# Optimization experiments

Hardware: AMD Instinct MI355X
Metric: run time of the kernel (lower is better)

## Reference

```python
import jax, jax.numpy as jnp
import numpy as np

IN_CHS = 128
NUM_HEADS = 4
WIN = 7
N = WIN * WIN            # 49 tokens per window
QKDIM = 128              # ceil(in_chs/num_groups/num_heads)*num_heads
HEAD_DIM = QKDIM // NUM_HEADS
SCALE = HEAD_DIM ** -0.5
B = 4096                 # batch * num_windows


def _relative_position_index(win_h, win_w):
    coords = np.stack(np.meshgrid(np.arange(win_h), np.arange(win_w), indexing='ij'))  # [2,h,w]
    cf = coords.reshape(2, -1)                      # [2, N]
    rc = (cf[:, :, None] - cf[:, None, :]).transpose(1, 2, 0).astype(np.int64)  # [N,N,2]
    rc[:, :, 0] += win_h - 1
    rc[:, :, 1] += win_w - 1
    rc[:, :, 0] *= 2 * win_w - 1
    return rc.sum(-1)                               # [N, N]


def setup_inputs() -> dict:
    key = jax.random.key(0)
    ks = jax.random.split(key, 8)
    x = jax.random.normal(ks[0], (B, N, IN_CHS), dtype=jnp.float32)
    qk_w = jax.random.normal(ks[1], (2 * QKDIM, IN_CHS), dtype=jnp.float32) * 0.02
    qk_b = jnp.zeros((2 * QKDIM,), dtype=jnp.float32)
    v_w = jax.random.normal(ks[2], (IN_CHS, IN_CHS), dtype=jnp.float32) * 0.02
    v_b = jnp.zeros((IN_CHS,), dtype=jnp.float32)
    proj_w = jax.random.normal(ks[3], (IN_CHS, IN_CHS), dtype=jnp.float32) * 0.02
    proj_b = jnp.zeros((IN_CHS,), dtype=jnp.float32)
    bias_table = jax.random.normal(ks[4], ((2 * WIN - 1) * (2 * WIN - 1), NUM_HEADS), dtype=jnp.float32) * 0.02
    rel_idx = jnp.asarray(_relative_position_index(WIN, WIN))  # [N,N] int64
    return {"x": x, "qk_w": qk_w, "qk_b": qk_b, "v_w": v_w, "v_b": v_b,
            "proj_w": proj_w, "proj_b": proj_b, "bias_table": bias_table,
            "rel_idx": rel_idx}


def reference(x, qk_w, qk_b, v_w, v_b, proj_w, proj_b, bias_table, rel_idx):
    Bn, Nn, C = x.shape
    # fused q/k projection: [B,N,2*qkdim] -> q,k each [B,H,N,d]
    qk = (x @ qk_w.T + qk_b).reshape(Bn, Nn, 2, NUM_HEADS, HEAD_DIM)
    q = qk[:, :, 0].transpose(0, 2, 1, 3)
    k = qk[:, :, 1].transpose(0, 2, 1, 3)
    v = (x @ v_w.T + v_b).reshape(Bn, Nn, NUM_HEADS, -1).transpose(0, 2, 1, 3)
    # windowed QK^T with gathered relative-position bias
    attn = jnp.einsum('bhnd,bhmd->bhnm', q * SCALE, k)
    bias = bias_table[rel_idx.reshape(-1)].reshape(Nn, Nn, NUM_HEADS).transpose(2, 0, 1)
    attn = jax.nn.softmax(attn + bias[None], axis=-1)
    out = jnp.einsum('bhnm,bhmd->bhnd', attn, v).transpose(0, 2, 1, 3).reshape(Bn, Nn, -1)
    return out @ proj_w.T + proj_b
```

## Files before the change

### kernel.cpp

```cpp
#include <hip/hip_runtime.h>
#include <hip/hip_bf16.h>

typedef __attribute__((ext_vector_type(8))) __bf16 bf16x8;
typedef __attribute__((ext_vector_type(4))) short short4v;
typedef __attribute__((ext_vector_type(4))) float f32x4;

#define MFMA(a,b,c) __builtin_amdgcn_mfma_f32_16x16x32_bf16((a),(b),(c),0,0,0)
#define MFMA16(a,b,c) __builtin_amdgcn_mfma_f32_16x16x16bf16_1k((a),(b),(c),0,0,0)

#define XB 0u
#define VT 16384u
#define OB 32768u

static __device__ __forceinline__ unsigned short f2u(float x) {
  return __builtin_bit_cast(unsigned short, static_cast<__bf16>(x));
}
static __device__ __forceinline__ unsigned long long pack4(float a, float b, float c, float d) {
  union { __bf16 h[4]; unsigned long long u; } z;
  z.h[0] = static_cast<__bf16>(a);
  z.h[1] = static_cast<__bf16>(b);
  z.h[2] = static_cast<__bf16>(c);
  z.h[3] = static_cast<__bf16>(d);
  return z.u;
}
static __device__ __forceinline__ unsigned long long pack4v(f32x4 v) {
  return pack4(v[0], v[1], v[2], v[3]);
}
static __device__ __forceinline__ short4v pack4s(float a, float b, float c, float d) {
  union { __bf16 h[4]; short4v s; } z;
  z.h[0] = static_cast<__bf16>(a);
  z.h[1] = static_cast<__bf16>(b);
  z.h[2] = static_cast<__bf16>(c);
  z.h[3] = static_cast<__bf16>(d);
  return z.s;
}
static __device__ __forceinline__ short4v pack4sv(f32x4 v) {
  return pack4s(v[0], v[1], v[2], v[3]);
}
static __device__ __forceinline__ unsigned sw256(unsigned row, unsigned colb) {
  return (row << 8) + (colb ^ ((row & 7u) << 4));
}
static __device__ __forceinline__ unsigned sw128(unsigned row, unsigned colb) {
  return (row << 7) + (colb ^ ((row & 7u) << 4));
}

__global__ void rsa_prep(const float* __restrict__ qk_w, const float* __restrict__ v_w,
                         const float* __restrict__ proj_w, const float* __restrict__ bias_table,
                         unsigned short* __restrict__ wqk, unsigned short* __restrict__ wv,
                         unsigned short* __restrict__ wp, float* __restrict__ biasNN) {
  const float QSCALE = 0.17677669529663687f * 1.4426950408889634f;
  const float LOG2E = 1.4426950408889634f;
  int t = blockIdx.x * blockDim.x + threadIdx.x;
  int stride = gridDim.x * blockDim.x;
  for (int i = t; i < 256 * 128; i += stride) {
    float v = qk_w[i];
    if (i < 128 * 128) v *= QSCALE;
    wqk[i] = f2u(v);
  }
  for (int i = t; i < 128 * 128; i += stride) wv[i] = f2u(v_w[i]);
  for (int i = t; i < 128 * 128; i += stride) wp[i] = f2u(proj_w[i]);
  for (int i = t; i < 4 * 64 * 64; i += stride) {
    int h = i >> 12, r = (i >> 6) & 63, m = i & 63;
    float v = -1e9f;
    if (r < 49 && m < 49) {
      int ri = r / 7, rj = r - ri * 7, mi = m / 7, mj = m - mi * 7;
      int rel = (ri - mi + 6) * 13 + (rj - mj + 6);
      v = bias_table[rel * 4 + h];
    }
    biasNN[i] = v * LOG2E;
  }
}

__global__ __launch_bounds__(256, 3) void rsa_main(
    const float* __restrict__ x, const float* __restrict__ qk_bias,
    const float* __restrict__ v_bias, const float* __restrict__ proj_bias,
    const unsigned short* __restrict__ wqk, const unsigned short* __restrict__ wv,
    const unsigned short* __restrict__ wp, const float* __restrict__ biasNN,
    float* __restrict__ out) {
  __shared__ __align__(16) unsigned char LDS[49152];
  const int tid = threadIdx.x;
  const int w = tid >> 6;
  const int lane = tid & 63;
  const int c = lane & 15;
  const int g = lane >> 4;
  const int b = blockIdx.x;
  const float QBSCALE = 0.17677669529663687f * 1.4426950408889634f;

  {
    const f32x4* xp = reinterpret_cast<const f32x4*>(x + (size_t)b * 6272);
    for (int i = tid; i < 1568; i += 256) {
      f32x4 v = xp[i];
      unsigned row = (unsigned)i >> 5, c4 = (unsigned)i & 31u;
      *reinterpret_cast<unsigned long long*>(LDS + XB + sw256(row, c4 * 8)) = pack4v(v);
    }
    for (int i = tid; i < 480; i += 256) {
      unsigned row = 49 + ((unsigned)i >> 5), c4 = (unsigned)i & 31u;
      *reinterpret_cast<unsigned long long*>(LDS + XB + sw256(row, c4 * 8)) = 0ull;
    }
  }
  __syncthreads();

  f32x4 qacc[2][4], kacc[2][4];
  {
#pragma unroll
    for (int kt = 0; kt < 2; ++kt) {
      f32x4 qb4 = *reinterpret_cast<const f32x4*>(qk_bias + (2 * w + kt) * 16 + g * 4);
      qb4[0] *= QBSCALE; qb4[1] *= QBSCALE; qb4[2] *= QBSCALE; qb4[3] *= QBSCALE;
      f32x4 kb4 = *reinterpret_cast<const f32x4*>(qk_bias + 128 + (2 * w + kt) * 16 + g * 4);
#pragma unroll
      for (int nt = 0; nt < 4; ++nt) { qacc[kt][nt] = qb4; kacc[kt][nt] = kb4; }
    }
    __builtin_amdgcn_s_setprio(1);
#pragma unroll
    for (int ks = 0; ks < 4; ++ks) {
      bf16x8 wq0 = *reinterpret_cast<const bf16x8*>(wqk + ((2 * w) * 16 + c) * 128 + ks * 32 + g * 8);
      bf16x8 wq1 = *reinterpret_cast<const bf16x8*>(wqk + ((2 * w + 1) * 16 + c) * 128 + ks * 32 + g * 8);
      bf16x8 wk0 = *reinterpret_cast<const bf16x8*>(wqk + (128 + (2 * w) * 16 + c) * 128 + ks * 32 + g * 8);
      bf16x8 wk1 = *reinterpret_cast<const bf16x8*>(wqk + (128 + (2 * w + 1) * 16 + c) * 128 + ks * 32 + g * 8);
#pragma unroll
      for (int nt = 0; nt < 4; ++nt) {
        bf16x8 xf = *reinterpret_cast<const bf16x8*>(LDS + XB + sw256(nt * 16 + c, (ks * 32 + g * 8) * 2));
        qacc[0][nt] = MFMA(wq0, xf, qacc[0][nt]);
        qacc[1][nt] = MFMA(wq1, xf, qacc[1][nt]);
        kacc[0][nt] = MFMA(wk0, xf, kacc[0][nt]);
        kacc[1][nt] = MFMA(wk1, xf, kacc[1][nt]);
      }
    }
    __builtin_amdgcn_s_setprio(0);
  }
  short4v q16[2][4], k16[2][4];
#pragma unroll
  for (int kt = 0; kt < 2; ++kt)
#pragma unroll
    for (int nt = 0; nt < 4; ++nt) {
      q16[kt][nt] = pack4sv(qacc[kt][nt]);
      k16[kt][nt] = pack4sv(kacc[kt][nt]);
    }

  __builtin_amdgcn_s_setprio(1);
#pragma unroll
  for (int ci = 0; ci < 2; ++ci) {
    const int ch = (2 * w + ci) * 16 + c;
    const float vb = v_bias[ch];
    f32x4 vacc[4];
#pragma unroll
    for (int mt = 0; mt < 4; ++mt) vacc[mt] = f32x4{vb, vb, vb, vb};
#pragma unroll
    for (int ks = 0; ks < 4; ++ks) {
      bf16x8 bw = *reinterpret_cast<const bf16x8*>(wv + ch * 128 + ks * 32 + g * 8);
#pragma unroll
      for (int mt = 0; mt < 4; ++mt) {
        bf16x8 xf = *reinterpret_cast<const bf16x8*>(LDS + XB + sw256(mt * 16 + c, (ks * 32 + g * 8) * 2));
        vacc[mt] = MFMA(xf, bw, vacc[mt]);
      }
    }
#pragma unroll
    for (int mt = 0; mt < 4; ++mt)
      *reinterpret_cast<unsigned long long*>(LDS + VT + sw128(ch, (mt * 16 + g * 4) * 2)) =
          pack4v(vacc[mt]);
  }
  __builtin_amdgcn_s_setprio(0);

  short4v pk[4][4];
#pragma unroll
  for (int rt = 0; rt < 4; ++rt) {
    f32x4 bbr[4];
    {
      const float* bp = biasNN + ((w * 64 + rt * 16 + c) << 6);
#pragma unroll
      for (int mt = 0; mt < 4; ++mt)
        bbr[mt] = *reinterpret_cast<const f32x4*>(bp + mt * 16 + g * 4);
    }
    f32x4 s[4];
    __builtin_amdgcn_s_setprio(1);
#pragma unroll
    for (int mt = 0; mt < 4; ++mt)
      s[mt] = MFMA16(k16[1][mt], q16[1][rt], MFMA16(k16[0][mt], q16[0][rt], bbr[mt]));
    __builtin_amdgcn_s_setprio(0);
    float v[16];
#pragma unroll
    for (int mt = 0; mt < 4; ++mt) {
#pragma unroll
      for (int j = 0; j < 4; ++j) v[mt * 4 + j] = exp2f(s[mt][j]);
    }
    float p0 = (v[0] + v[1]) + (v[2] + v[3]);
    float p1 = (v[4] + v[5]) + (v[6] + v[7]);
    float p2 = (v[8] + v[9]) + (v[10] + v[11]);
    float p3 = (v[12] + v[13]) + (v[14] + v[15]);
    float sum = (p0 + p1) + (p2 + p3);
    sum += __shfl_xor(sum, 16);
    sum += __shfl_xor(sum, 32);
    const float inv = __builtin_amdgcn_rcpf(sum);
#pragma unroll
    for (int mt = 0; mt < 4; ++mt)
      pk[rt][mt] = pack4s(v[mt * 4] * inv, v[mt * 4 + 1] * inv,
                          v[mt * 4 + 2] * inv, v[mt * 4 + 3] * inv);
  }

  f32x4 od[2][4];
  {
    short4v vfrag[2][4];
#pragma unroll
    for (int ct = 0; ct < 2; ++ct)
#pragma unroll
      for (int mt = 0; mt < 4; ++mt)
        vfrag[ct][mt] = *reinterpret_cast<const short4v*>(
            LDS + VT + sw128((2 * w + ct) * 16 + c, (mt * 16 + g * 4) * 2));
#pragma unroll
    for (int ct = 0; ct < 2; ++ct)
#pragma unroll
      for (int rt = 0; rt < 4; ++rt) od[ct][rt] = f32x4{0.f, 0.f, 0.f, 0.f};
    __builtin_amdgcn_s_setprio(1);
#pragma unroll
    for (int mt = 0; mt < 4; ++mt)
#pragma unroll
      for (int ct = 0; ct < 2; ++ct)
#pragma unroll
        for (int rt = 0; rt < 4; ++rt)
          od[ct][rt] = MFMA16(vfrag[ct][mt], pk[rt][mt], od[ct][rt]);
    __builtin_amdgcn_s_setprio(0);
  }

  bf16x8 ap[2][4];
  f32x4 pb4[2];
#pragma unroll
  for (int u = 0; u < 2; ++u) {
    const unsigned short* wrow = wp + ((2 * w + u) * 16 + c) * 128 + g * 8;
#pragma unroll
    for (int ks = 0; ks < 4; ++ks) ap[u][ks] = *reinterpret_cast<const bf16x8*>(wrow + ks * 32);
    pb4[u] = *reinterpret_cast<const f32x4*>(proj_bias + (2 * w + u) * 16 + g * 4);
  }

#pragma unroll
  for (int ct = 0; ct < 2; ++ct)
#pragma unroll
    for (int rt = 0; rt < 4; ++rt)
      *reinterpret_cast<unsigned long long*>(
          LDS + OB + sw256(rt * 16 + c, ((2 * w + ct) * 16 + g * 4) * 2)) = pack4v(od[ct][rt]);
  __syncthreads();

  __builtin_amdgcn_s_setprio(1);
#pragma unroll
  for (int u = 0; u < 2; ++u) {
    f32x4 acc[4];
#pragma unroll
    for (int nt = 0; nt < 4; ++nt) acc[nt] = pb4[u];
#pragma unroll
    for (int ks = 0; ks < 4; ++ks) {
#pragma unroll
      for (int nt = 0; nt < 4; ++nt) {
        bf16x8 bf = *reinterpret_cast<const bf16x8*>(LDS + OB + sw256(nt * 16 + c, (ks * 32 + g * 8) * 2));
        acc[nt] = MFMA(ap[u][ks], bf, acc[nt]);
      }
    }
#pragma unroll
    for (int nt = 0; nt < 4; ++nt) {
      const int tok = nt * 16 + c;
      if (tok < 49) {
        *reinterpret_cast<f32x4*>(out + ((size_t)b * 49 + tok) * 128 + (2 * w + u) * 16 + g * 4) = acc[nt];
      }
    }
  }
  __builtin_amdgcn_s_setprio(0);
}

extern "C" void kernel_launch(void* const* d_in, const int* in_sizes, int n_in,
                              void* d_out, int out_size, void* d_ws, size_t ws_size,
                              hipStream_t stream) {
  const float* x          = (const float*)d_in[0];
  const float* qk_w       = (const float*)d_in[1];
  const float* qk_b       = (const float*)d_in[2];
  const float* v_w        = (const float*)d_in[3];
  const float* v_b        = (const float*)d_in[4];
  const float* proj_w     = (const float*)d_in[5];
  const float* proj_b     = (const float*)d_in[6];
  const float* bias_table = (const float*)d_in[7];
  float* out = (float*)d_out;

  unsigned short* wqk = (unsigned short*)d_ws;
  unsigned short* wv  = wqk + 256 * 128;
  unsigned short* wp  = wv + 128 * 128;
  float* biasNN = (float*)((char*)d_ws + 131072);

  const int B = in_sizes[0] / (49 * 128);

  rsa_prep<<<dim3(128), dim3(512), 0, stream>>>(qk_w, v_w, proj_w, bias_table, wqk, wv, wp, biasNN);
  rsa_main<<<dim3(B), dim3(256), 0, stream>>>(x, qk_b, v_b, proj_b, wqk, wv, wp, biasNN, out);
}
```

Baseline: 122.3 us.

## Process two windows per 512-thread block and alias output buffer onto x region

Each block now handles two windows with eight waves (four per window), doubling block size and using 64KB LDS. The post-attention output tile is written into the window's own x staging region instead of a separate buffer, with an extra block barrier added after the V store. This is meant to cut per-block launch and setup overhead and raise LDS-limited occupancy. The cost is the extra barrier and coupling two windows' progress through shared syncs.

```diff
diff --git a/kernel.cpp b/kernel.cpp
--- a/kernel.cpp
+++ b/kernel.cpp
@@ -9,8 +9,7 @@
 #define MFMA16(a,b,c) __builtin_amdgcn_mfma_f32_16x16x16bf16_1k((a),(b),(c),0,0,0)
 
 #define XB 0u
-#define VT 16384u
-#define OB 32768u
+#define VT 32768u
 
 static __device__ __forceinline__ unsigned short f2u(float x) {
   return __builtin_bit_cast(unsigned short, static_cast<__bf16>(x));
@@ -71,55 +70,67 @@
   }
 }
 
-__global__ __launch_bounds__(256, 3) void rsa_main(
+__global__ __launch_bounds__(512, 4) void rsa_main(
     const float* __restrict__ x, const float* __restrict__ qk_bias,
     const float* __restrict__ v_bias, const float* __restrict__ proj_bias,
     const unsigned short* __restrict__ wqk, const unsigned short* __restrict__ wv,
     const unsigned short* __restrict__ wp, const float* __restrict__ biasNN,
-    float* __restrict__ out) {
-  __shared__ __align__(16) unsigned char LDS[49152];
+    float* __restrict__ out, int Btot) {
+  __shared__ __align__(16) unsigned char LDS[65536];
   const int tid = threadIdx.x;
   const int w = tid >> 6;
   const int lane = tid & 63;
   const int c = lane & 15;
   const int g = lane >> 4;
-  const int b = blockIdx.x;
+  const int wi = w >> 2;
+  const int h = w & 3;
   const float QBSCALE = 0.17677669529663687f * 1.4426950408889634f;
 
+  const int b0 = blockIdx.x * 2;
+  const int bmine = b0 + wi;
+
   {
-    const f32x4* xp = reinterpret_cast<const f32x4*>(x + (size_t)b * 6272);
-    for (int i = tid; i < 1568; i += 256) {
-      f32x4 v = xp[i];
-      unsigned row = (unsigned)i >> 5, c4 = (unsigned)i & 31u;
-      *reinterpret_cast<unsigned long long*>(LDS + XB + sw256(row, c4 * 8)) = pack4v(v);
-    }
-    for (int i = tid; i < 480; i += 256) {
-      unsigned row = 49 + ((unsigned)i >> 5), c4 = (unsigned)i & 31u;
-      *reinterpret_cast<unsigned long long*>(LDS + XB + sw256(row, c4 * 8)) = 0ull;
+#pragma unroll
+    for (int s2 = 0; s2 < 2; ++s2) {
+      const int bb = (b0 + s2 < Btot) ? b0 + s2 : b0;
+      const f32x4* xp = reinterpret_cast<const f32x4*>(x + (size_t)bb * 6272);
+      const unsigned base = XB + (unsigned)s2 * 16384u;
+      for (int i = tid; i < 1568; i += 512) {
+        f32x4 v = xp[i];
+        unsigned row = (unsigned)i >> 5, c4 = (unsigned)i & 31u;
+        *reinterpret_cast<unsigned long long*>(LDS + base + sw256(row, c4 * 8)) = pack4v(v);
+      }
+      for (int i = tid; i < 480; i += 512) {
+        unsigned row = 49 + ((unsigned)i >> 5), c4 = (unsigned)i & 31u;
+        *reinterpret_cast<unsigned long long*>(LDS + base + sw256(row, c4 * 8)) = 0ull;
+      }
     }
   }
   __syncthreads();
+
+  const unsigned XW = XB + (unsigned)wi * 16384u;
+  const unsigned VW = VT + (unsigned)wi * 16384u;
 
   f32x4 qacc[2][4], kacc[2][4];
   {
 #pragma unroll
     for (int kt = 0; kt < 2; ++kt) {
-      f32x4 qb4 = *reinterpret_cast<const f32x4*>(qk_bias + (2 * w + kt) * 16 + g * 4);
+      f32x4 qb4 = *reinterpret_cast<const f32x4*>(qk_bias + (2 * h + kt) * 16 + g * 4);
       qb4[0] *= QBSCALE; qb4[1] *= QBSCALE; qb4[2] *= QBSCALE; qb4[3] *= QBSCALE;
-      f32x4 kb4 = *reinterpret_cast<const f32x4*>(qk_bias + 128 + (2 * w + kt) * 16 + g * 4);
+      f32x4 kb4 = *reinterpret_cast<const f32x4*>(qk_bias + 128 + (2 * h + kt) * 16 + g * 4);
 #pragma unroll
       for (int nt = 0; nt < 4; ++nt) { qacc[kt][nt] = qb4; kacc[kt][nt] = kb4; }
     }
     __builtin_amdgcn_s_setprio(1);
 #pragma unroll
     for (int ks = 0; ks < 4; ++ks) {
-      bf16x8 wq0 = *reinterpret_cast<const bf16x8*>(wqk + ((2 * w) * 16 + c) * 128 + ks * 32 + g * 8);
-      bf16x8 wq1 = *reinterpret_cast<const bf16x8*>(wqk + ((2 * w + 1) * 16 + c) * 128 + ks * 32 + g * 8);
-      bf16x8 wk0 = *reinterpret_cast<const bf16x8*>(wqk + (128 + (2 * w) * 16 + c) * 128 + ks * 32 + g * 8);
-      bf16x8 wk1 = *reinterpret_cast<const bf16x8*>(wqk + (128 + (2 * w + 1) * 16 + c) * 128 + ks * 32 + g * 8);
+      bf16x8 wq0 = *reinterpret_cast<const bf16x8*>(wqk + ((2 * h) * 16 + c) * 128 + ks * 32 + g * 8);
+      bf16x8 wq1 = *reinterpret_cast<const bf16x8*>(wqk + ((2 * h + 1) * 16 + c) * 128 + ks * 32 + g * 8);
+      bf16x8 wk0 = *reinterpret_cast<const bf16x8*>(wqk + (128 + (2 * h) * 16 + c) * 128 + ks * 32 + g * 8);
+      bf16x8 wk1 = *reinterpret_cast<const bf16x8*>(wqk + (128 + (2 * h + 1) * 16 + c) * 128 + ks * 32 + g * 8);
 #pragma unroll
       for (int nt = 0; nt < 4; ++nt) {
-        bf16x8 xf = *reinterpret_cast<const bf16x8*>(LDS + XB + sw256(nt * 16 + c, (ks * 32 + g * 8) * 2));
+        bf16x8 xf = *reinterpret_cast<const bf16x8*>(LDS + XW + sw256(nt * 16 + c, (ks * 32 + g * 8) * 2));
         qacc[0][nt] = MFMA(wq0, xf, qacc[0][nt]);
         qacc[1][nt] = MFMA(wq1, xf, qacc[1][nt]);
         kacc[0][nt] = MFMA(wk0, xf, kacc[0][nt]);
@@ -140,7 +151,7 @@
   __builtin_amdgcn_s_setprio(1);
 #pragma unroll
   for (int ci = 0; ci < 2; ++ci) {
-    const int ch = (2 * w + ci) * 16 + c;
+    const int ch = (2 * h + ci) * 16 + c;
     const float vb = v_bias[ch];
     f32x4 vacc[4];
 #pragma unroll
@@ -150,23 +161,24 @@
       bf16x8 bw = *reinterpret_cast<const bf16x8*>(wv + ch * 128 + ks * 32 + g * 8);
 #pragma unroll
       for (int mt = 0; mt < 4; ++mt) {
-        bf16x8 xf = *reinterpret_cast<const bf16x8*>(LDS + XB + sw256(mt * 16 + c, (ks * 32 + g * 8) * 2));
+        bf16x8 xf = *reinterpret_cast<const bf16x8*>(LDS + XW + sw256(mt * 16 + c, (ks * 32 + g * 8) * 2));
         vacc[mt] = MFMA(xf, bw, vacc[mt]);
       }
     }
 #pragma unroll
     for (int mt = 0; mt < 4; ++mt)
-      *reinterpret_cast<unsigned long long*>(LDS + VT + sw128(ch, (mt * 16 + g * 4) * 2)) =
+      *reinterpret_cast<unsigned long long*>(LDS + VW + sw128(ch, (mt * 16 + g * 4) * 2)) =
           pack4v(vacc[mt]);
   }
   __builtin_amdgcn_s_setprio(0);
+  __syncthreads();
 
   short4v pk[4][4];
 #pragma unroll
   for (int rt = 0; rt < 4; ++rt) {
     f32x4 bbr[4];
     {
-      const float* bp = biasNN + ((w * 64 + rt * 16 + c) << 6);
+      const float* bp = biasNN + ((h * 64 + rt * 16 + c) << 6);
 #pragma unroll
       for (int mt = 0; mt < 4; ++mt)
         bbr[mt] = *reinterpret_cast<const f32x4*>(bp + mt * 16 + g * 4);
@@ -205,7 +217,7 @@
 #pragma unroll
       for (int mt = 0; mt < 4; ++mt)
         vfrag[ct][mt] = *reinterpret_cast<const short4v*>(
-            LDS + VT + sw128((2 * w + ct) * 16 + c, (mt * 16 + g * 4) * 2));
+            LDS + VW + sw128((2 * h + ct) * 16 + c, (mt * 16 + g * 4) * 2));
 #pragma unroll
     for (int ct = 0; ct < 2; ++ct)
 #pragma unroll
@@ -225,10 +237,10 @@
   f32x4 pb4[2];
 #pragma unroll
   for (int u = 0; u < 2; ++u) {
-    const unsigned short* wrow = wp + ((2 * w + u) * 16 + c) * 128 + g * 8;
+    const unsigned short* wrow = wp + ((2 * h + u) * 16 + c) * 128 + g * 8;
 #pragma unroll
     for (int ks = 0; ks < 4; ++ks) ap[u][ks] = *reinterpret_cast<const bf16x8*>(wrow + ks * 32);
-    pb4[u] = *reinterpret_cast<const f32x4*>(proj_bias + (2 * w + u) * 16 + g * 4);
+    pb4[u] = *reinterpret_cast<const f32x4*>(proj_bias + (2 * h + u) * 16 + g * 4);
   }
 
 #pragma unroll
@@ -236,32 +248,34 @@
 #pragma unroll
     for (int rt = 0; rt < 4; ++rt)
       *reinterpret_cast<unsigned long long*>(
-          LDS + OB + sw256(rt * 16 + c, ((2 * w + ct) * 16 + g * 4) * 2)) = pack4v(od[ct][rt]);
+          LDS + XW + sw256(rt * 16 + c, ((2 * h + ct) * 16 + g * 4) * 2)) = pack4v(od[ct][rt]);
   __syncthreads();
 
-  __builtin_amdgcn_s_setprio(1);
-#pragma unroll
-  for (int u = 0; u < 2; ++u) {
-    f32x4 acc[4];
-#pragma unroll
-    for (int nt = 0; nt < 4; ++nt) acc[nt] = pb4[u];
-#pragma unroll
-    for (int ks = 0; ks < 4; ++ks) {
+  if (bmine < Btot) {
+    __builtin_amdgcn_s_setprio(1);
+#pragma unroll
+    for (int u = 0; u < 2; ++u) {
+      f32x4 acc[4];
+#pragma unroll
+      for (int nt = 0; nt < 4; ++nt) acc[nt] = pb4[u];
+#pragma unroll
+      for (int ks = 0; ks < 4; ++ks) {
+#pragma unroll
+        for (int nt = 0; nt < 4; ++nt) {
+          bf16x8 bf = *reinterpret_cast<const bf16x8*>(LDS + XW + sw256(nt * 16 + c, (ks * 32 + g * 8) * 2));
+          acc[nt] = MFMA(ap[u][ks], bf, acc[nt]);
+        }
+      }
 #pragma unroll
       for (int nt = 0; nt < 4; ++nt) {
-        bf16x8 bf = *reinterpret_cast<const bf16x8*>(LDS + OB + sw256(nt * 16 + c, (ks * 32 + g * 8) * 2));
-        acc[nt] = MFMA(ap[u][ks], bf, acc[nt]);
-      }
-    }
-#pragma unroll
-    for (int nt = 0; nt < 4; ++nt) {
-      const int tok = nt * 16 + c;
-      if (tok < 49) {
-        *reinterpret_cast<f32x4*>(out + ((size_t)b * 49 + tok) * 128 + (2 * w + u) * 16 + g * 4) = acc[nt];
-      }
-    }
-  }
-  __builtin_amdgcn_s_setprio(0);
+        const int tok = nt * 16 + c;
+        if (tok < 49) {
+          *reinterpret_cast<f32x4*>(out + ((size_t)bmine * 49 + tok) * 128 + (2 * h + u) * 16 + g * 4) = acc[nt];
+        }
+      }
+    }
+    __builtin_amdgcn_s_setprio(0);
+  }
 }
 
 extern "C" void kernel_launch(void* const* d_in, const int* in_sizes, int n_in,
@@ -283,7 +297,8 @@
   float* biasNN = (float*)((char*)d_ws + 131072);
 
   const int B = in_sizes[0] / (49 * 128);
-
-  rsa_prep<<<dim3(128), dim3(512), 0, stream>>>(qk_w, v_w, proj_w, bias_table, wqk, wv, wp, biasNN);
-  rsa_main<<<dim3(B), dim3(256), 0, stream>>>(x, qk_b, v_b, proj_b, wqk, wv, wp, biasNN, out);
-}
+  const int grid = (B + 1) / 2;
+
+  rsa_prep<<<dim3(256), dim3(512), 0, stream>>>(qk_w, v_w, proj_w, bias_table, wqk, wv, wp, biasNN);
+  rsa_main<<<dim3(grid), dim3(512), 0, stream>>>(x, qk_b, v_b, proj_b, wqk, wv, wp, biasNN, out, B);
+}
```

Result: slower. 126.8 us (+3.7%).
